# Kernel optimization log

Hardware: AMD Instinct MI355X
Metric: run time of the kernel (lower is better)

The kernel has to match this reference:

```python
import jax, jax.numpy as jnp
import numpy as np

H = 32        # query heads
KV = 8        # kv heads
HD = 128      # head_dim
EPS = 1e-6
THETA = 1e6
T = 2048
D = 4096


def _rms_norm(x, w):
    # x: [T, heads, HD]
    var = jnp.mean(jnp.square(x), axis=-1, keepdims=True)
    return x * jax.lax.rsqrt(var + EPS) * w


def _rope(x, cos, sin):
    # NEOX-style rotary: split last dim in halves. x: [T, heads, HD]
    x1, x2 = jnp.split(x, 2, axis=-1)
    return jnp.concatenate([x1 * cos - x2 * sin, x2 * cos + x1 * sin], axis=-1)


def setup_inputs() -> dict:
    key = jax.random.key(0)
    k1, k2, k3 = jax.random.split(key, 3)
    s = 1.0 / np.sqrt(D)
    return {
        "positions": jnp.arange(T, dtype=jnp.int32),
        "hidden_states": jax.random.normal(k1, (T, D), dtype=jnp.float32),
        "w_qkv": jax.random.normal(k2, (D, (H + 2 * KV) * HD), dtype=jnp.float32) * s,
        "q_norm_w": jnp.ones((HD,), dtype=jnp.float32),
        "k_norm_w": jnp.ones((HD,), dtype=jnp.float32),
        "w_o": jax.random.normal(k3, (H * HD, D), dtype=jnp.float32) * s,
    }


def reference(positions, hidden_states, w_qkv, q_norm_w, k_norm_w, w_o):
    scale = HD ** -0.5
    qkv = hidden_states @ w_qkv                              # [T, (H+2KV)*HD]
    q = qkv[:, : H * HD].reshape(T, H, HD)
    k = qkv[:, H * HD : (H + KV) * HD].reshape(T, KV, HD)
    v = qkv[:, (H + KV) * HD :].reshape(T, KV, HD)

    # per-head RMSNorm on q/k (Qwen3 QK-norm)
    q = _rms_norm(q, q_norm_w)
    k = _rms_norm(k, k_norm_w)

    # RoPE
    inv_freq = 1.0 / (THETA ** (jnp.arange(0, HD, 2, dtype=jnp.float32) / HD))
    freqs = positions.astype(jnp.float32)[:, None] * inv_freq  # [T, HD/2]
    cos = jnp.cos(freqs)[:, None, :]                            # [T, 1, HD/2]
    sin = jnp.sin(freqs)[:, None, :]
    q = _rope(q, cos, sin)
    k = _rope(k, cos, sin)

    # GQA: repeat kv heads
    rep = H // KV
    k = jnp.repeat(k, rep, axis=1)                           # [T, H, HD]
    v = jnp.repeat(v, rep, axis=1)

    # causal SDPA
    scores = jnp.einsum("thd,shd->hts", q, k) * scale        # [H, T, T]
    causal = jnp.tril(jnp.ones((T, T), dtype=bool))
    scores = jnp.where(causal[None], scores, jnp.finfo(scores.dtype).min)
    probs = jax.nn.softmax(scores, axis=-1)
    attn = jnp.einsum("hts,shd->thd", probs, v).reshape(T, H * HD)

    return attn @ w_o                                        # [T, D]
```

## Files before the change

### kernel.cpp

```cpp
#include <hip/hip_runtime.h>

#define TT   2048
#define DD   4096
#define NH   32
#define NKVH 8
#define HDM  128
#define KD   4096
#define NQKV 6144

typedef unsigned short u16;
typedef short v8s __attribute__((ext_vector_type(8)));
typedef float v4f __attribute__((ext_vector_type(4)));

#define QSCALE 0.12751744547734565f
#define EOFF   17.312340490667562f
#define CTS 390

__device__ __forceinline__ u16 f2bf(float f) {
    unsigned u = __builtin_bit_cast(unsigned, f);
    u += 0x7fffu + ((u >> 16) & 1u);
    return (u16)(u >> 16);
}
__device__ __forceinline__ float bf2f(u16 h) {
    return __builtin_bit_cast(float, ((unsigned)h) << 16);
}
__device__ __forceinline__ void gl2lds16(const void* g, void* l) {
    using gv = const __attribute__((address_space(1))) void;
    using lv = __attribute__((address_space(3))) void;
    __builtin_amdgcn_global_load_lds((gv*)g, (lv*)l, 16, 0, 0);
}

__device__ __forceinline__ void transpose_tile64(const float* __restrict__ in,
                                                 u16* __restrict__ out,
                                                 int K, int N, int n0, int k0,
                                                 float* tile, int t) {
    int rc = t >> 4, cc = (t & 15) * 4;
#pragma unroll
    for (int p = 0; p < 4; ++p) {
        int k = p * 16 + rc;
        float4 v = *(const float4*)&in[(size_t)(k0 + k) * N + n0 + cc];
        tile[k * 65 + cc] = v.x; tile[k * 65 + cc + 1] = v.y;
        tile[k * 65 + cc + 2] = v.z; tile[k * 65 + cc + 3] = v.w;
    }
    __syncthreads();
    int rn = t >> 3, ck = (t & 7) * 8;
#pragma unroll
    for (int p = 0; p < 2; ++p) {
        int n = p * 32 + rn;
        v8s tv;
#pragma unroll
        for (int j = 0; j < 8; ++j) tv[j] = (short)f2bf(tile[(ck + j) * 65 + n]);
        *(v8s*)&out[(size_t)(n0 + n) * K + k0 + ck] = tv;
    }
}

__global__ __launch_bounds__(256) void prep_all_kernel(const float* __restrict__ hidden,
                                                       u16* __restrict__ hid_bf,
                                                       const int* __restrict__ positions,
                                                       float* __restrict__ cosT,
                                                       float* __restrict__ sinT,
                                                       const float* __restrict__ w_qkv,
                                                       u16* __restrict__ wqkv_t) {
    __shared__ float tile[64 * 65];
    int b = blockIdx.x;
    if (b < 4096) {
        size_t i = ((size_t)b * 256 + threadIdx.x) * 8;
        float4 a = *(const float4*)&hidden[i];
        float4 c = *(const float4*)&hidden[i + 4];
        v8s tv;
        tv[0] = (short)f2bf(a.x); tv[1] = (short)f2bf(a.y);
        tv[2] = (short)f2bf(a.z); tv[3] = (short)f2bf(a.w);
        tv[4] = (short)f2bf(c.x); tv[5] = (short)f2bf(c.y);
        tv[6] = (short)f2bf(c.z); tv[7] = (short)f2bf(c.w);
        *(v8s*)&hid_bf[i] = tv;
    } else if (b < 4608) {
        int idx = (b - 4096) * 256 + threadIdx.x;
        int tp = idx >> 6, i = idx & 63;
        float invf = exp2f(-(float)i * 0.31143075889569023f);
        float f = (float)positions[tp] * invf;
        cosT[idx] = cosf(f);
        sinT[idx] = sinf(f);
    } else {
        int bx = b - 4608;
        int n0 = (bx % 96) * 64, k0 = (bx / 96) * 64;
        transpose_tile64(w_qkv, wqkv_t, 4096, NQKV, n0, k0, tile, threadIdx.x);
    }
}

__global__ __launch_bounds__(512, 2) void gemm_out_kernel(
    const u16* __restrict__ A, const u16* __restrict__ Bt, float* __restrict__ C)
{
    __shared__ __align__(16) char smem_raw[98304];
    u16* lds = (u16*)smem_raw;
    const int tid = threadIdx.x;
    const int wave = tid >> 6, lane = tid & 63;
    const int quad = lane >> 4, l15 = lane & 15, lm = l15 & 7;
    const int wm = wave >> 2, wn = wave & 3;
    const int m0 = blockIdx.y * 128, n0 = blockIdx.x * 256;

    v4f acc[4][4];
    v4f z4 = {0.f, 0.f, 0.f, 0.f};
#pragma unroll
    for (int mi = 0; mi < 4; ++mi)
#pragma unroll
        for (int ni = 0; ni < 4; ++ni) acc[mi][ni] = z4;

    const int rsub = lane >> 3;
    const int cg = (lane & 7) ^ rsub;
    const int ch0a = wave * 2, ch0b = wave * 4;
    const int g0 = (quad ^ lm) << 3;
    const int g1 = ((4 + quad) ^ lm) << 3;

    const u16* AgR0 = &A[((size_t)m0 + (ch0a + 0) * 8 + rsub) * KD + cg * 8];
    const u16* AgR1 = &A[((size_t)m0 + (ch0a + 1) * 8 + rsub) * KD + cg * 8];
    const u16* BgR0 = &Bt[((size_t)n0 + (ch0b + 0) * 8 + rsub) * KD + cg * 8];
    const u16* BgR1 = &Bt[((size_t)n0 + (ch0b + 1) * 8 + rsub) * KD + cg * 8];
    const u16* BgR2 = &Bt[((size_t)n0 + (ch0b + 2) * 8 + rsub) * KD + cg * 8];
    const u16* BgR3 = &Bt[((size_t)n0 + (ch0b + 3) * 8 + rsub) * KD + cg * 8];

#define OSTAGE(tt) do { \
    int _b = ((tt) & 1) * 24576; \
    gl2lds16(AgR0 + (size_t)(tt) * 64, &lds[_b + (ch0a + 0) * 512]); \
    gl2lds16(AgR1 + (size_t)(tt) * 64, &lds[_b + (ch0a + 1) * 512]); \
    gl2lds16(BgR0 + (size_t)(tt) * 64, &lds[_b + 8192 + (ch0b + 0) * 512]); \
    gl2lds16(BgR1 + (size_t)(tt) * 64, &lds[_b + 8192 + (ch0b + 1) * 512]); \
    gl2lds16(BgR2 + (size_t)(tt) * 64, &lds[_b + 8192 + (ch0b + 2) * 512]); \
    gl2lds16(BgR3 + (size_t)(tt) * 64, &lds[_b + 8192 + (ch0b + 3) * 512]); \
  } while (0)

    v8s af[4], bfr[4];

#define OPHASE(BO, G, STAGE_CODE, WAIT_CODE) do { \
    _Pragma("unroll") \
    for (int mi = 0; mi < 4; ++mi) \
        af[mi] = *(const v8s*)&lds[(BO) + (wm * 64 + mi * 16 + l15) * 64 + (G)]; \
    _Pragma("unroll") \
    for (int ni = 0; ni < 4; ++ni) \
        bfr[ni] = *(const v8s*)&lds[(BO) + 8192 + (wn * 64 + ni * 16 + l15) * 64 + (G)]; \
    STAGE_CODE; \
    __builtin_amdgcn_s_barrier(); \
    asm volatile("" ::: "memory"); \
    __builtin_amdgcn_s_setprio(1); \
    _Pragma("unroll") \
    for (int mi = 0; mi < 4; ++mi) \
      _Pragma("unroll") \
      for (int ni = 0; ni < 4; ++ni) \
        acc[mi][ni] = __builtin_amdgcn_mfma_f32_16x16x32_bf16( \
            af[mi], bfr[ni], acc[mi][ni], 0, 0, 0); \
    __builtin_amdgcn_s_setprio(0); \
    WAIT_CODE; \
    __builtin_amdgcn_s_barrier(); \
  } while (0)

#define VM0 asm volatile("s_waitcnt vmcnt(0)" ::: "memory")

    OSTAGE(0);
    VM0;
    __builtin_amdgcn_s_barrier();

#pragma unroll 2
    for (int t = 0; t < 62; ++t) {
        const int bo = (t & 1) * 24576;
        OPHASE(bo, g0, { OSTAGE(t + 1); }, {});
        OPHASE(bo, g1, {}, { VM0; });
    }
    OPHASE(0, g0, { OSTAGE(63); }, {});
    OPHASE(0, g1, {}, { VM0; });
    OPHASE(24576, g0, {}, {});
    OPHASE(24576, g1, {}, {});
#undef OPHASE
#undef OSTAGE
#undef VM0

#pragma unroll
    for (int mi = 0; mi < 4; ++mi)
#pragma unroll
        for (int ni = 0; ni < 4; ++ni)
#pragma unroll
            for (int r = 0; r < 4; ++r)
                C[(size_t)(m0 + wm * 64 + mi * 16 + quad * 4 + r) * 4096 +
                  (n0 + wn * 64 + ni * 16 + l15)] = acc[mi][ni][r];
}

__global__ __launch_bounds__(512, 2) void gemm_qkv384_kernel(
    const u16* __restrict__ A, const u16* __restrict__ Bt,
    const float* __restrict__ qw, const float* __restrict__ kw,
    const float* __restrict__ cosT, const float* __restrict__ sinT,
    u16* __restrict__ Qb, u16* __restrict__ Kb, u16* __restrict__ Vt)
{
    __shared__ __align__(16) char smem_raw[131072];
    u16* lds = (u16*)smem_raw;
    const int tid = threadIdx.x;
    const int wave = tid >> 6, lane = tid & 63;
    const int quad = lane >> 4, l15 = lane & 15, lm = l15 & 7;
    const int wm = wave >> 2, wn = wave & 3;
    const int m0 = blockIdx.y * 128, n0 = blockIdx.x * 384;

    v4f acc[2][4][3];
    v4f z4 = {0.f, 0.f, 0.f, 0.f};
#pragma unroll
    for (int nh = 0; nh < 2; ++nh)
#pragma unroll
        for (int mi = 0; mi < 4; ++mi)
#pragma unroll
            for (int ni = 0; ni < 3; ++ni) acc[nh][mi][ni] = z4;

    const int rsub = lane >> 3;
    const int cg = (lane & 7) ^ rsub;
    const int ch0 = wave * 2;
    const int g0 = (quad ^ lm) << 3;
    const int g1 = ((4 + quad) ^ lm) << 3;

    const u16* AgR0 = &A[((size_t)m0 + (ch0 + 0) * 8 + rsub) * KD + cg * 8];
    const u16* AgR1 = &A[((size_t)m0 + (ch0 + 1) * 8 + rsub) * KD + cg * 8];
    const u16* BgR0 = &Bt[((size_t)n0 + (ch0 + 0) * 8 + rsub) * KD + cg * 8];
    const u16* BgR1 = &Bt[((size_t)n0 + (ch0 + 1) * 8 + rsub) * KD + cg * 8];

#define STAGE_AH(tt) do { \
    int _b = ((tt) & 1) * 32768; \
    gl2lds16(AgR0 + (size_t)(tt) * 64, &lds[_b + (ch0 + 0) * 512]); \
    gl2lds16(AgR1 + (size_t)(tt) * 64, &lds[_b + (ch0 + 1) * 512]); \
  } while (0)
#define STAGE_BH(tt, h) do { \
    int _b = ((tt) & 1) * 32768 + 8192; \
    gl2lds16(BgR0 + (size_t)(h) * 128 * KD + (size_t)(tt) * 64, \
             &lds[_b + (h) * 8192 + (ch0 + 0) * 512]); \
    gl2lds16(BgR1 + (size_t)(h) * 128 * KD + (size_t)(tt) * 64, \
             &lds[_b + (h) * 8192 + (ch0 + 1) * 512]); \
  } while (0)

    v8s af[4], bfr[3];

#define PHASEX(BO, G, NHI, RDA, STAGE_CODE, WAIT_CODE) do { \
    if (RDA) { \
      _Pragma("unroll") \
      for (int mi = 0; mi < 4; ++mi) \
        af[mi] = *(const v8s*)&lds[(BO) + (wm * 64 + mi * 16 + l15) * 64 + (G)]; \
    } \
    _Pragma("unroll") \
    for (int ni = 0; ni < 3; ++ni) \
      bfr[ni] = *(const v8s*)&lds[(BO) + 8192 + \
                   (wn * 96 + (NHI) * 48 + ni * 16 + l15) * 64 + (G)]; \
    STAGE_CODE; \
    __builtin_amdgcn_s_barrier(); \
    asm volatile("" ::: "memory"); \
    __builtin_amdgcn_s_setprio(1); \
    _Pragma("unroll") \
    for (int mi = 0; mi < 4; ++mi) \
      _Pragma("unroll") \
      for (int ni = 0; ni < 3; ++ni) \
        acc[NHI][mi][ni] = __builtin_amdgcn_mfma_f32_16x16x32_bf16( \
            af[mi], bfr[ni], acc[NHI][mi][ni], 0, 0, 0); \
    __builtin_amdgcn_s_setprio(0); \
    WAIT_CODE; \
    __builtin_amdgcn_s_barrier(); \
  } while (0)

#define VM0 asm volatile("s_waitcnt vmcnt(0)" ::: "memory")

#define TILE_MAIN(BO, TT1) do { \
    PHASEX(BO, g0, 0, 1, { STAGE_AH(TT1); STAGE_BH(TT1, 0); }, {}); \
    PHASEX(BO, g0, 1, 0, { STAGE_BH(TT1, 1); }, {}); \
    PHASEX(BO, g1, 0, 1, { STAGE_BH(TT1, 2); }, {}); \
    PHASEX(BO, g1, 1, 0, {}, { VM0; }); \
  } while (0)

    STAGE_AH(0); STAGE_BH(0, 0); STAGE_BH(0, 1); STAGE_BH(0, 2);
    VM0;
    __builtin_amdgcn_s_barrier();

#pragma unroll 2
    for (int t = 0; t < 62; ++t) {
        const int bo = (t & 1) * 32768;
        TILE_MAIN(bo, t + 1);
    }
    TILE_MAIN(0, 63);
    PHASEX(32768, g0, 0, 1, {}, {});
    PHASEX(32768, g0, 1, 0, {}, {});
    PHASEX(32768, g1, 0, 1, {}, {});
    PHASEX(32768, g1, 1, 0, {}, {});
#undef TILE_MAIN
#undef PHASEX
#undef STAGE_AH
#undef STAGE_BH
#undef VM0

    u16* Ct = lds;
    const int t0q = blockIdx.y * 128;
    __syncthreads();
#pragma unroll
    for (int nh = 0; nh < 2; ++nh)
#pragma unroll
        for (int mi = 0; mi < 4; ++mi)
#pragma unroll
            for (int ni = 0; ni < 3; ++ni)
#pragma unroll
                for (int r = 0; r < 4; ++r)
                    Ct[(wm * 64 + mi * 16 + quad * 4 + r) * CTS +
                       wn * 96 + nh * 48 + ni * 16 + l15] = f2bf(acc[nh][mi][ni][r]);
    __syncthreads();
    if (tid < 384) {
        const int row = tid & 127, hh = tid >> 7;
        const int head = blockIdx.x * 3 + hh;
        if (head < 40) {
            const float* w = (head < 32) ? qw : kw;
            float ss = 0.f;
            for (int i = 0; i < 128; ++i) {
                float x = bf2f(Ct[row * CTS + hh * 128 + i]);
                ss += x * x;
            }
            float rs = rsqrtf(ss * (1.0f / 128.0f) + 1e-6f);
            if (head < 32) rs *= QSCALE;
            const int ti = t0q + row;
            for (int i = 0; i < 64; ++i) {
                float x1 = bf2f(Ct[row * CTS + hh * 128 + i]) * rs * w[i];
                float x2 = bf2f(Ct[row * CTS + hh * 128 + 64 + i]) * rs * w[64 + i];
                float c = cosT[ti * 64 + i], s = sinT[ti * 64 + i];
                Ct[row * CTS + hh * 128 + i]      = f2bf(x1 * c - x2 * s);
                Ct[row * CTS + hh * 128 + 64 + i] = f2bf(x2 * c + x1 * s);
            }
        }
    }
    __syncthreads();
#pragma unroll
    for (int hh = 0; hh < 3; ++hh) {
        const int head = blockIdx.x * 3 + hh;
        if (head < 40) {
            u16* dst = (head < 32) ? &Qb[((size_t)head * TT + t0q) * HDM]
                                   : &Kb[((size_t)(head - 32) * TT + t0q) * HDM];
            for (int cix = tid; cix < 128 * 16; cix += 512) {
                int row = cix >> 4, part = (cix & 15) * 8;
                v8s tv;
#pragma unroll
                for (int j = 0; j < 8; ++j) tv[j] = (short)Ct[row * CTS + hh * 128 + part + j];
                *(v8s*)&dst[row * HDM + part] = tv;
            }
        } else {
            const int kvh = head - 40;
            for (int cix = tid; cix < 128 * 16; cix += 512) {
                int hd = cix & 127, tb = cix >> 7;
                v8s tv;
#pragma unroll
                for (int j = 0; j < 8; ++j) tv[j] = (short)Ct[(tb * 8 + j) * CTS + hh * 128 + hd];
                *(v8s*)&Vt[((size_t)kvh * HDM + hd) * TT + t0q + tb * 8] = tv;
            }
        }
    }
}

__global__ __launch_bounds__(256) void attn_plus_kernel(
    const u16* __restrict__ Qb, const u16* __restrict__ Kb,
    const u16* __restrict__ Vt, u16* __restrict__ Ob,
    const float* __restrict__ w_o, u16* __restrict__ wo_t)
{
    __shared__ __align__(16) char smem_raw[40960];
    int tid = threadIdx.x;
    if (blockIdx.x >= 1024) {
        int bx = blockIdx.x - 1024;
        int n0 = (bx & 63) * 64, k0 = (bx >> 6) * 64;
        transpose_tile64(w_o, wo_t, 4096, 4096, n0, k0, (float*)smem_raw, tid);
        return;
    }
    u16* Kl = (u16*)smem_raw;
    u16* Vl = (u16*)(smem_raw + 16384);
    u16* Pl = (u16*)(smem_raw + 32768);
    int wave = tid >> 6, lane = tid & 63;
    int quad = lane >> 4, l15 = lane & 15;
    int idx = blockIdx.x;
    int h = idx & 31;
    int qb = 31 - (idx >> 5);
    int kv = h >> 2;
    int q0 = qb * 64;
    int lm = l15 & 7;

    v8s qf[4];
    {
        const u16* qr = &Qb[((size_t)h * TT + q0 + wave * 16 + l15) * HDM];
#pragma unroll
        for (int ks = 0; ks < 4; ++ks) qf[ks] = *(const v8s*)&qr[ks * 32 + quad * 8];
    }

    v4f z4 = {0.f, 0.f, 0.f, 0.f};
    v4f of[8];
#pragma unroll
    for (int i = 0; i < 8; ++i) of[i] = z4;
    float lsum[4];
#pragma unroll
    for (int r = 0; r < 4; ++r) lsum[r] = 0.f;
    u16* Pw = &Pl[wave * 1024];

    for (int s0 = 0; s0 <= q0; s0 += 64) {
        __syncthreads();
#pragma unroll
        for (int c = 0; c < 4; ++c) {
            int ch = wave * 4 + c;
            int rk = ch * 4 + (lane >> 4);
            int ck = (lane & 15) ^ (rk & 7);
            gl2lds16(&Kb[((size_t)kv * TT + s0 + rk) * HDM + ck * 8], &Kl[ch * 512]);
            int rv = ch * 8 + (lane >> 3);
            int cv = (lane & 7) ^ (rv & 7);
            gl2lds16(&Vt[((size_t)kv * HDM + rv) * TT + s0 + cv * 8], &Vl[ch * 512]);
        }
        __syncthreads();
        v4f sf[4];
#pragma unroll
        for (int nt = 0; nt < 4; ++nt) {
            v4f cacc = z4;
#pragma unroll
            for (int ks = 0; ks < 4; ++ks)
                cacc = __builtin_amdgcn_mfma_f32_16x16x32_bf16(
                    qf[ks],
                    *(const v8s*)&Kl[(nt * 16 + l15) * 128 + (((ks * 4 + quad) ^ lm) << 3)],
                    cacc, 0, 0, 0);
            sf[nt] = cacc;
        }
        if (s0 == q0) {
#pragma unroll
            for (int nt = 0; nt < 4; ++nt) {
                int sg = s0 + nt * 16 + l15;
#pragma unroll
                for (int r = 0; r < 4; ++r) {
                    int qg = q0 + wave * 16 + quad * 4 + r;
                    if (sg > qg) sf[nt][r] = -3.0e38f;
                }
            }
        }
#pragma unroll
        for (int nt = 0; nt < 4; ++nt)
#pragma unroll
            for (int r = 0; r < 4; ++r) {
                float p = exp2f(sf[nt][r] - EOFF);
                sf[nt][r] = p;
                lsum[r] += p;
            }
#pragma unroll
        for (int nt = 0; nt < 4; ++nt)
#pragma unroll
            for (int r = 0; r < 4; ++r) {
                int row = quad * 4 + r;
                int pch = ((nt << 1) + (l15 >> 3)) ^ (row & 7);
                Pw[row * 64 + pch * 8 + (l15 & 7)] = f2bf(sf[nt][r]);
            }
#pragma unroll
        for (int sub = 0; sub < 2; ++sub) {
            v8s pa = *(const v8s*)&Pw[l15 * 64 + ((((sub << 2) + quad) ^ lm) << 3)];
#pragma unroll
            for (int nt = 0; nt < 8; ++nt)
                of[nt] = __builtin_amdgcn_mfma_f32_16x16x32_bf16(
                    pa,
                    *(const v8s*)&Vl[(nt * 16 + l15) * 64 + ((((sub << 2) + quad) ^ lm) << 3)],
                    of[nt], 0, 0, 0);
        }
    }
#pragma unroll
    for (int off = 1; off < 16; off <<= 1)
#pragma unroll
        for (int r = 0; r < 4; ++r) lsum[r] += __shfl_xor(lsum[r], off, 64);
    float invl[4];
#pragma unroll
    for (int r = 0; r < 4; ++r) invl[r] = 1.0f / lsum[r];
#pragma unroll
    for (int nt = 0; nt < 8; ++nt)
#pragma unroll
        for (int r = 0; r < 4; ++r)
            Ob[(size_t)(q0 + wave * 16 + quad * 4 + r) * (NH * HDM) + h * HDM + nt * 16 + l15] =
                f2bf(of[nt][r] * invl[r]);
}

extern "C" void kernel_launch(void* const* d_in, const int* in_sizes, int n_in,
                              void* d_out, int out_size, void* d_ws, size_t ws_size,
                              hipStream_t stream)
{
    (void)in_sizes; (void)n_in; (void)out_size; (void)ws_size;
    const int*   positions = (const int*)d_in[0];
    const float* hidden    = (const float*)d_in[1];
    const float* w_qkv     = (const float*)d_in[2];
    const float* q_norm_w  = (const float*)d_in[3];
    const float* k_norm_w  = (const float*)d_in[4];
    const float* w_o       = (const float*)d_in[5];
    float* out = (float*)d_out;
    char* ws = (char*)d_ws;
    char* ob = (char*)d_out;

    u16* hid_bf = (u16*)(ws + 0);
    u16* attnO  = (u16*)(ws + 0);
    u16* wqkv_t = (u16*)(ws + (size_t)16777216);
    u16* wo_t   = (u16*)(ws + (size_t)16777216);

    u16*   Qb   = (u16*)(ob + 0);
    u16*   Kb   = (u16*)(ob + (size_t)16777216);
    u16*   Vt   = (u16*)(ob + (size_t)20971520);
    float* cosT = (float*)(ob + (size_t)25165824);
    float* sinT = (float*)(ob + (size_t)25690112);

    prep_all_kernel<<<10752, 256, 0, stream>>>(hidden, hid_bf, positions, cosT, sinT,
                                               w_qkv, wqkv_t);

    gemm_qkv384_kernel<<<dim3(16, 16), 512, 0, stream>>>(
        hid_bf, wqkv_t, q_norm_w, k_norm_w, cosT, sinT, Qb, Kb, Vt);

    attn_plus_kernel<<<5120, 256, 0, stream>>>(Qb, Kb, Vt, attnO, w_o, wo_t);

    gemm_out_kernel<<<dim3(16, 16), 512, 0, stream>>>(attnO, wo_t, out);
}
```

Measured before the change: 451.3 us.

## Collapse multi-phase GEMM k-loops into single-barrier tiles with batched fragment loads

Both GEMM kernels (output projection and QKV) drop their ping-pong phase structure, in which each k-tile was split into 2 or 4 phases with two barriers each and setprio toggling. Each k-tile now issues all global-to-LDS stages up front and loads both k-halves of the A/B fragments at once. It then runs all MFMAs and ends with a single vmcnt wait and barrier. This cuts barrier count and scheduling overhead, at the cost of more live fragment registers and less explicit interleaving of LDS reads with MFMA work.

```diff
diff --git a/kernel.cpp b/kernel.cpp
--- a/kernel.cpp
+++ b/kernel.cpp
@@ -128,31 +128,35 @@
     gl2lds16(BgR3 + (size_t)(tt) * 64, &lds[_b + 8192 + (ch0b + 3) * 512]); \
   } while (0)
 
-    v8s af[4], bfr[4];
-
-#define OPHASE(BO, G, STAGE_CODE, WAIT_CODE) do { \
+#define VM0 asm volatile("s_waitcnt vmcnt(0)" ::: "memory")
+
+#define OTILE(BO, STAGE_CODE) do { \
+    STAGE_CODE; \
+    v8s af0[4], af1[4], bf0[4], bf1[4]; \
     _Pragma("unroll") \
-    for (int mi = 0; mi < 4; ++mi) \
-        af[mi] = *(const v8s*)&lds[(BO) + (wm * 64 + mi * 16 + l15) * 64 + (G)]; \
+    for (int mi = 0; mi < 4; ++mi) { \
+        const u16* ap = &lds[(BO) + (wm * 64 + mi * 16 + l15) * 64]; \
+        af0[mi] = *(const v8s*)&ap[g0]; \
+        af1[mi] = *(const v8s*)&ap[g1]; \
+    } \
     _Pragma("unroll") \
-    for (int ni = 0; ni < 4; ++ni) \
-        bfr[ni] = *(const v8s*)&lds[(BO) + 8192 + (wn * 64 + ni * 16 + l15) * 64 + (G)]; \
-    STAGE_CODE; \
-    __builtin_amdgcn_s_barrier(); \
-    asm volatile("" ::: "memory"); \
-    __builtin_amdgcn_s_setprio(1); \
+    for (int ni = 0; ni < 4; ++ni) { \
+        const u16* bp = &lds[(BO) + 8192 + (wn * 64 + ni * 16 + l15) * 64]; \
+        bf0[ni] = *(const v8s*)&bp[g0]; \
+        bf1[ni] = *(const v8s*)&bp[g1]; \
+    } \
     _Pragma("unroll") \
     for (int mi = 0; mi < 4; ++mi) \
       _Pragma("unroll") \
-      for (int ni = 0; ni < 4; ++ni) \
+      for (int ni = 0; ni < 4; ++ni) { \
         acc[mi][ni] = __builtin_amdgcn_mfma_f32_16x16x32_bf16( \
-            af[mi], bfr[ni], acc[mi][ni], 0, 0, 0); \
-    __builtin_amdgcn_s_setprio(0); \
-    WAIT_CODE; \
+            af0[mi], bf0[ni], acc[mi][ni], 0, 0, 0); \
+        acc[mi][ni] = __builtin_amdgcn_mfma_f32_16x16x32_bf16( \
+            af1[mi], bf1[ni], acc[mi][ni], 0, 0, 0); \
+      } \
+    VM0; \
     __builtin_amdgcn_s_barrier(); \
   } while (0)
-
-#define VM0 asm volatile("s_waitcnt vmcnt(0)" ::: "memory")
 
     OSTAGE(0);
     VM0;
@@ -161,14 +165,11 @@
 #pragma unroll 2
     for (int t = 0; t < 62; ++t) {
         const int bo = (t & 1) * 24576;
-        OPHASE(bo, g0, { OSTAGE(t + 1); }, {});
-        OPHASE(bo, g1, {}, { VM0; });
-    }
-    OPHASE(0, g0, { OSTAGE(63); }, {});
-    OPHASE(0, g1, {}, { VM0; });
-    OPHASE(24576, g0, {}, {});
-    OPHASE(24576, g1, {}, {});
-#undef OPHASE
+        OTILE(bo, { OSTAGE(t + 1); });
+    }
+    OTILE(0, { OSTAGE(63); });
+    OTILE(24576, {});
+#undef OTILE
 #undef OSTAGE
 #undef VM0
 
@@ -229,40 +230,38 @@
              &lds[_b + (h) * 8192 + (ch0 + 1) * 512]); \
   } while (0)
 
-    v8s af[4], bfr[3];
-
-#define PHASEX(BO, G, NHI, RDA, STAGE_CODE, WAIT_CODE) do { \
-    if (RDA) { \
+#define VM0 asm volatile("s_waitcnt vmcnt(0)" ::: "memory")
+
+#define TILE_BODY(BO, STAGE_CODE) do { \
+    STAGE_CODE; \
+    v8s af0[4], af1[4], bf0[2][3], bf1[2][3]; \
+    _Pragma("unroll") \
+    for (int mi = 0; mi < 4; ++mi) { \
+        const u16* ap = &lds[(BO) + (wm * 64 + mi * 16 + l15) * 64]; \
+        af0[mi] = *(const v8s*)&ap[g0]; \
+        af1[mi] = *(const v8s*)&ap[g1]; \
+    } \
+    _Pragma("unroll") \
+    for (int nh = 0; nh < 2; ++nh) \
+      _Pragma("unroll") \
+      for (int ni = 0; ni < 3; ++ni) { \
+        const u16* bp = &lds[(BO) + 8192 + (wn * 96 + nh * 48 + ni * 16 + l15) * 64]; \
+        bf0[nh][ni] = *(const v8s*)&bp[g0]; \
+        bf1[nh][ni] = *(const v8s*)&bp[g1]; \
+      } \
+    _Pragma("unroll") \
+    for (int nh = 0; nh < 2; ++nh) \
       _Pragma("unroll") \
       for (int mi = 0; mi < 4; ++mi) \
-        af[mi] = *(const v8s*)&lds[(BO) + (wm * 64 + mi * 16 + l15) * 64 + (G)]; \
-    } \
-    _Pragma("unroll") \
-    for (int ni = 0; ni < 3; ++ni) \
-      bfr[ni] = *(const v8s*)&lds[(BO) + 8192 + \
-                   (wn * 96 + (NHI) * 48 + ni * 16 + l15) * 64 + (G)]; \
-    STAGE_CODE; \
+        _Pragma("unroll") \
+        for (int ni = 0; ni < 3; ++ni) { \
+          acc[nh][mi][ni] = __builtin_amdgcn_mfma_f32_16x16x32_bf16( \
+              af0[mi], bf0[nh][ni], acc[nh][mi][ni], 0, 0, 0); \
+          acc[nh][mi][ni] = __builtin_amdgcn_mfma_f32_16x16x32_bf16( \
+              af1[mi], bf1[nh][ni], acc[nh][mi][ni], 0, 0, 0); \
+        } \
+    VM0; \
     __builtin_amdgcn_s_barrier(); \
-    asm volatile("" ::: "memory"); \
-    __builtin_amdgcn_s_setprio(1); \
-    _Pragma("unroll") \
-    for (int mi = 0; mi < 4; ++mi) \
-      _Pragma("unroll") \
-      for (int ni = 0; ni < 3; ++ni) \
-        acc[NHI][mi][ni] = __builtin_amdgcn_mfma_f32_16x16x32_bf16( \
-            af[mi], bfr[ni], acc[NHI][mi][ni], 0, 0, 0); \
-    __builtin_amdgcn_s_setprio(0); \
-    WAIT_CODE; \
-    __builtin_amdgcn_s_barrier(); \
-  } while (0)
-
-#define VM0 asm volatile("s_waitcnt vmcnt(0)" ::: "memory")
-
-#define TILE_MAIN(BO, TT1) do { \
-    PHASEX(BO, g0, 0, 1, { STAGE_AH(TT1); STAGE_BH(TT1, 0); }, {}); \
-    PHASEX(BO, g0, 1, 0, { STAGE_BH(TT1, 1); }, {}); \
-    PHASEX(BO, g1, 0, 1, { STAGE_BH(TT1, 2); }, {}); \
-    PHASEX(BO, g1, 1, 0, {}, { VM0; }); \
   } while (0)
 
     STAGE_AH(0); STAGE_BH(0, 0); STAGE_BH(0, 1); STAGE_BH(0, 2);
@@ -272,15 +271,12 @@
 #pragma unroll 2
     for (int t = 0; t < 62; ++t) {
         const int bo = (t & 1) * 32768;
-        TILE_MAIN(bo, t + 1);
-    }
-    TILE_MAIN(0, 63);
-    PHASEX(32768, g0, 0, 1, {}, {});
-    PHASEX(32768, g0, 1, 0, {}, {});
-    PHASEX(32768, g1, 0, 1, {}, {});
-    PHASEX(32768, g1, 1, 0, {}, {});
-#undef TILE_MAIN
-#undef PHASEX
+        TILE_BODY(bo, { STAGE_AH(t + 1); STAGE_BH(t + 1, 0);
+                        STAGE_BH(t + 1, 1); STAGE_BH(t + 1, 2); });
+    }
+    TILE_BODY(0, { STAGE_AH(63); STAGE_BH(63, 0); STAGE_BH(63, 1); STAGE_BH(63, 2); });
+    TILE_BODY(32768, {});
+#undef TILE_BODY
 #undef STAGE_AH
 #undef STAGE_BH
 #undef VM0
```

Measured after the change: 439.2 us. 2.7% less time.
